# Performance work log

Hardware: AMD Instinct MI355X
Metric: run time of the kernel (lower is better)

Reference implementation:

```python
import jax, jax.numpy as jnp
import numpy as np


def setup_inputs() -> dict:
    key = jax.random.key(0)
    ks = jax.random.split(key, 6)
    Ci, Co, m1, m2 = 64, 64, 32, 32
    B, S = 16, 256
    inp = {
        "x": jax.random.normal(ks[0], (B, Ci, S, S), dtype=jnp.float32),
        "y0_r": jax.random.normal(ks[1], (Ci, Co, m1 - 1, 1), dtype=jnp.float32) * 0.02,
        "y0_i": jax.random.normal(ks[2], (Ci, Co, m1 - 1, 1), dtype=jnp.float32) * 0.02,
        "yposx_r": jax.random.normal(ks[3], (Ci, Co, 2 * m1 - 1, m2 - 1), dtype=jnp.float32) * 0.02,
        "yposx_i": jax.random.normal(ks[4], (Ci, Co, 2 * m1 - 1, m2 - 1), dtype=jnp.float32) * 0.02,
        "w00": jax.random.normal(ks[5], (Ci, Co, 1, 1), dtype=jnp.float32) * 0.02,
        "out_size": 256,
    }
    return inp


def _build_weights(y0_r, y0_i, yposx_r, yposx_i, w00):
    # torch: cat([y0, w00.cfloat(), y0.flip(-2).conj()], dim=-2) then cat with yposx on dim=-1
    y0 = y0_r + 1j * y0_i                      # [Ci,Co,m1-1,1]
    yposx = yposx_r + 1j * yposx_i             # [Ci,Co,2m1-1,m2-1]
    col0 = jnp.concatenate(
        [y0, w00.astype(jnp.complex64), jnp.conj(jnp.flip(y0, axis=-2))], axis=-2
    )                                           # [Ci,Co,2m1-1,1]
    return jnp.concatenate([col0, yposx], axis=-1)  # [Ci,Co,2m1-1,m2]


def reference(x, y0_r, y0_i, yposx_r, yposx_i, w00, out_size):
    m1 = y0_r.shape[-2] + 1
    m2 = yposx_r.shape[-1] + 1
    Co = y0_r.shape[1]
    B = x.shape[0]
    in_size = x.shape[-1]
    H = x.shape[-2]
    weights = _build_weights(y0_r, y0_i, yposx_r, yposx_i, w00)

    # index of zero frequency after fftshift (== N//2 for fftfreq of length N)
    f0_in = H // 2
    x_ft = jnp.fft.fftshift(jnp.fft.rfft2(x, norm="ortho"), axes=-2)
    x_ft = x_ft[..., f0_in - m1 + 1 : f0_in + m1, :m2]       # [B,Ci,2m1-1,m2]

    out_modes = jnp.einsum("bixy,ioxy->boxy", x_ft, weights)  # [B,Co,2m1-1,m2]

    f0_out = out_size // 2
    out_ft = jnp.zeros((B, Co, out_size, out_size // 2 + 1), dtype=jnp.complex64)
    out_ft = out_ft.at[..., f0_out - m1 + 1 : f0_out + m1, :m2].set(out_modes)

    y = jnp.fft.irfft2(
        jnp.fft.ifftshift(out_ft, axes=-2), s=(out_size, out_size), norm="ortho"
    ) * (out_size / in_size)
    return y.astype(jnp.float32)
```

## Files before the change

### kernel.cpp

```cpp
#include <hip/hip_runtime.h>


typedef __attribute__((ext_vector_type(8))) short bfrag8;
typedef __attribute__((ext_vector_type(4))) float facc4;

#define F1F_O 0u
#define T2F_O 16384u
#define T4F_O 81920u
#define F5F_O 147456u
#define WF_O  163840u
#define X1T_O 33193984u
#define C2_O  49971200u
#define X2M_O 54165504u
#define WTMP_O WF_O
#define C3_O  X1T_O
#define X3T_O (X1T_O + 4128768u)

#define TWO_PI_256 0.0245436926f

__device__ __forceinline__ unsigned short f2bf(float f) {
  unsigned u = __float_as_uint(f);
  u += 0x7fffu + ((u >> 16) & 1u);
  return (unsigned short)(u >> 16);
}
__device__ __forceinline__ bfrag8 ldf(const unsigned short* p) {
  return *(const bfrag8*)p;
}
__device__ __forceinline__ bfrag8 ld8u2(const unsigned short* p) {
  union { uint2 u2[2]; bfrag8 f; } v;
  v.u2[0] = *(const uint2*)(p);
  v.u2[1] = *(const uint2*)(p + 4);
  return v.f;
}

__global__ void k_tables(unsigned short* ws) {
  int t = threadIdx.x;
  for (int q = 0; q < 4; ++q) {
    int idx = blockIdx.x * 1024 + q * 256 + t;
    float val = 0.f; unsigned dst;
    if (idx < 16384) {
      int u = idx, j = u & 7, lane = (u >> 3) & 63, nt = (u >> 9) & 3, ks = u >> 11;
      int k = ks * 32 + (lane >> 4) * 8 + j, n = nt * 16 + (lane & 15);
      if (n < 32) val =  cosf((float)((k * n) & 255) * TWO_PI_256) * (1.f / 256.f);
      else        val = -sinf((float)((k * (n - 32)) & 255) * TWO_PI_256) * (1.f / 256.f);
      dst = F1F_O + (unsigned)idx;
    } else if (idx < 81920) {
      int u = idx - 16384, j = u & 7, lane = (u >> 3) & 63, ks = (u >> 9) & 15, mt = u >> 13;
      int m = mt * 16 + (lane & 15), k = ks * 32 + (lane >> 4) * 8 + j;
      if (m < 126) {
        int ky = m < 63 ? m : m - 63;
        int y = k & 255, f = (ky + 225) & 255;
        float ang = (float)((y * f) & 255) * TWO_PI_256;
        float c = cosf(ang), s = sinf(ang);
        val = (m < 63) ? ((k < 256) ? c : s) : ((k < 256) ? -s : c);
      }
      dst = T2F_O + (unsigned)u;
    } else if (idx < 147456) {
      int u = idx - 81920, j = u & 7, lane = (u >> 3) & 63, ks = (u >> 9) & 3, mt = u >> 11;
      int m = mt * 16 + (lane & 15), k = ks * 32 + (lane >> 4) * 8 + j;
      if (k < 126) {
        int ky = k < 63 ? k : k - 63;
        int y = m & 255, f = (ky + 225) & 255;
        float ang = (float)((y * f) & 255) * TWO_PI_256;
        float c = cosf(ang), s = sinf(ang);
        val = (m < 256) ? ((k < 63) ? c : -s) : ((k < 63) ? s : c);
      }
      dst = T4F_O + (unsigned)u;
    } else {
      int u = idx - 147456, j = u & 7, lane = (u >> 3) & 63, nt = (u >> 9) & 15, ks = u >> 13;
      int k = ks * 32 + (lane >> 4) * 8 + j, n = nt * 16 + (lane & 15);
      int kf = k & 31;
      float ang = (float)((kf * n) & 255) * TWO_PI_256;
      if (k < 32) val = ((kf == 0) ? 1.f : 2.f) * cosf(ang) * (1.f / 256.f);
      else        val = (kf == 0) ? 0.f : -2.f * sinf(ang) * (1.f / 256.f);
      dst = F5F_O + (unsigned)u;
    }
    ws[dst] = f2bf(val);
  }
}

__global__ void k_wpre(const float* __restrict__ y0r, const float* __restrict__ y0i,
                       const float* __restrict__ ypr, const float* __restrict__ ypi,
                       const float* __restrict__ w00, unsigned short* ws) {
  unsigned* Wtmp = (unsigned*)(ws + WTMP_O);
  int chunk = blockIdx.x >> 4, kq = blockIdx.x & 15;
  int io = chunk * 256 + threadIdx.x;
  int ky0 = kq * 4, nky = (kq == 15) ? 3 : 4;
  const float* pr = ypr + (size_t)io * 1953 + (size_t)ky0 * 31;
  const float* pi_ = ypi + (size_t)io * 1953 + (size_t)ky0 * 31;
  for (int q = 0; q < nky; ++q) {
    int ky = ky0 + q;
#pragma unroll
    for (int kxs = 0; kxs < 31; ++kxs) {
      float r = pr[q * 31 + kxs], im = pi_[q * 31 + kxs];
      Wtmp[(unsigned)(ky * 32 + kxs + 1) * 4096u + io] =
          (unsigned)f2bf(r) | ((unsigned)f2bf(im) << 16);
    }
  }
  if (kq == 0) {
    float rr[31], ii[31];
#pragma unroll
    for (int j = 0; j < 31; ++j) { rr[j] = y0r[io * 31 + j]; ii[j] = y0i[io * 31 + j]; }
    float w0 = w00[io];
    for (int ky = 0; ky < 63; ++ky) {
      float r, im;
      if (ky < 31)       { r = rr[ky];      im = ii[ky]; }
      else if (ky == 31) { r = w0;          im = 0.f; }
      else               { r = rr[62 - ky]; im = -ii[62 - ky]; }
      Wtmp[(unsigned)(ky * 32) * 4096u + io] =
          (unsigned)f2bf(r) | ((unsigned)f2bf(im) << 16);
    }
  }
}

__global__ void k_s1(const float* __restrict__ x, unsigned short* ws) {
  __shared__ unsigned short F1s[16384];
  __shared__ unsigned short As[128 * 40];
  const unsigned short* F1g = ws + F1F_O;
  unsigned short* X1t = ws + X1T_O;
  int t = threadIdx.x;
  int bi = blockIdx.x >> 1, y0 = (blockIdx.x & 1) * 128;
#pragma unroll
  for (int q = 0; q < 8; ++q)
    ((uint4*)F1s)[q * 256 + t] = ((const uint4*)F1g)[q * 256 + t];
  int lane = t & 63, w = t >> 6, quad = lane >> 4, nlo = lane & 15;
  int mt0 = w * 2;
  facc4 acc[2][4];
#pragma unroll
  for (int a = 0; a < 2; ++a)
#pragma unroll
    for (int b = 0; b < 4; ++b) acc[a][b] = (facc4){0.f, 0.f, 0.f, 0.f};
  const float* img = x + (size_t)bi * 65536 + (size_t)y0 * 256;
  for (int ks = 0; ks < 8; ++ks) {
    __syncthreads();
#pragma unroll
    for (int q = 0; q < 4; ++q) {
      int flat = q * 1024 + t * 4;
      int r = flat >> 5, cc = flat & 31;
      float4 v = *(const float4*)(img + r * 256 + ks * 32 + cc);
      unsigned short b4[4] = { f2bf(v.x), f2bf(v.y), f2bf(v.z), f2bf(v.w) };
      *(uint2*)(As + r * 40 + cc) = *(uint2*)b4;
    }
    __syncthreads();
    bfrag8 a0 = *(bfrag8*)(As + (mt0 * 16 + nlo) * 40 + quad * 8);
    bfrag8 a1 = *(bfrag8*)(As + ((mt0 + 1) * 16 + nlo) * 40 + quad * 8);
#pragma unroll
    for (int nt = 0; nt < 4; ++nt) {
      bfrag8 b = *(bfrag8*)(F1s + ((ks * 4 + nt) * 64 + lane) * 8);
      acc[0][nt] = __builtin_amdgcn_mfma_f32_16x16x32_bf16(a0, b, acc[0][nt], 0, 0, 0);
      acc[1][nt] = __builtin_amdgcn_mfma_f32_16x16x32_bf16(a1, b, acc[1][nt], 0, 0, 0);
    }
  }
#pragma unroll
  for (int ml = 0; ml < 2; ++ml)
#pragma unroll
    for (int nt = 0; nt < 4; ++nt) {
      facc4 v = acc[ml][nt];
      int ccol = nt * 16 + nlo, n = ccol & 31, half = ccol >> 5;
      int yrow = y0 + (mt0 + ml) * 16 + quad * 4;
      unsigned short pk[4] = { f2bf(v[0]), f2bf(v[1]), f2bf(v[2]), f2bf(v[3]) };
      *(uint2*)(X1t + (unsigned)bi * 16384u + n * 512 + half * 256 + yrow) = *(uint2*)pk;
    }
}

__global__ void k_s2(unsigned short* ws) {
  const unsigned short* T2f = ws + T2F_O;
  const unsigned short* X1t = ws + X1T_O;
  unsigned short* C2 = ws + C2_O;
  int t = threadIdx.x, lane = t & 63, w = t >> 6, quad = lane >> 4, nlo = lane & 15;
  int bi = blockIdx.x, mt0 = w * 2;
  facc4 acc[2][2];
#pragma unroll
  for (int a = 0; a < 2; ++a)
#pragma unroll
    for (int b = 0; b < 2; ++b) acc[a][b] = (facc4){0.f, 0.f, 0.f, 0.f};
  const unsigned short* Bb = X1t + (unsigned)bi * 16384u;
  for (int ks = 0; ks < 16; ++ks) {
    bfrag8 a0 = ldf(T2f + ((mt0 * 16 + ks) * 64 + lane) * 8);
    bfrag8 a1 = ldf(T2f + (((mt0 + 1) * 16 + ks) * 64 + lane) * 8);
    bfrag8 b0 = ldf(Bb + nlo * 512 + ks * 32 + quad * 8);
    bfrag8 b1 = ldf(Bb + (16 + nlo) * 512 + ks * 32 + quad * 8);
    acc[0][0] = __builtin_amdgcn_mfma_f32_16x16x32_bf16(a0, b0, acc[0][0], 0, 0, 0);
    acc[0][1] = __builtin_amdgcn_mfma_f32_16x16x32_bf16(a0, b1, acc[0][1], 0, 0, 0);
    acc[1][0] = __builtin_amdgcn_mfma_f32_16x16x32_bf16(a1, b0, acc[1][0], 0, 0, 0);
    acc[1][1] = __builtin_amdgcn_mfma_f32_16x16x32_bf16(a1, b1, acc[1][1], 0, 0, 0);
  }
#pragma unroll
  for (int ml = 0; ml < 2; ++ml)
#pragma unroll
    for (int nt = 0; nt < 2; ++nt) {
      facc4 v = acc[ml][nt];
      int n = nt * 16 + nlo, mb = (mt0 + ml) * 16 + quad * 4;
#pragma unroll
      for (int r = 0; r < 4; ++r)
        C2[(unsigned)bi * 4096u + (mb + r) * 32 + n] = f2bf(v[r]);
    }
}

__global__ void k_t1(unsigned short* ws) {
  __shared__ unsigned short lds[512 * 36];
  const unsigned short* C2 = ws + C2_O;
  unsigned short* X2m = ws + X2M_O;
  int ky = blockIdx.x >> 2, b0 = (blockIdx.x & 3) * 4;
  int t = threadIdx.x;
#pragma unroll
  for (int rr = 0; rr < 2; ++rr) {
    int R = rr * 256 + t;
    int half = R >> 8, bloc = (R >> 6) & 3, i = R & 63;
    const uint2* src2 = (const uint2*)(C2 + (unsigned)((b0 + bloc) * 64 + i) * 4096u
                                          + (half * 63 + ky) * 32);
    uint2* d2 = (uint2*)(lds + R * 36);
#pragma unroll
    for (int c = 0; c < 8; ++c) d2[c] = src2[c];
  }
  __syncthreads();
#pragma unroll
  for (int it = 0; it < 8; ++it) {
    int flat = (it * 256 + t) * 8;
    int kx = flat >> 9, bloc = (flat >> 7) & 3, ic0 = flat & 127;
    unsigned short outv[8];
#pragma unroll
    for (int j = 0; j < 8; ++j) {
      int ic = ic0 + j, i = ic & 63, half = ic >> 6;
      outv[j] = lds[(half * 256 + bloc * 64 + i) * 36 + kx];
    }
    *(uint4*)(X2m + (unsigned)(ky * 32 + kx) * 2048u + (b0 + bloc) * 128 + ic0) = *(uint4*)outv;
  }
}

__global__ void k_s3(unsigned short* ws) {
  __shared__ unsigned lds[64 * 65];
  const unsigned short* X2m = ws + X2M_O;
  const unsigned* Wtmp = (const unsigned*)(ws + WTMP_O);
  unsigned short* C3 = ws + C3_O;
  int t = threadIdx.x, lane = t & 63, w = t >> 6, quad = lane >> 4, nlo = lane & 15;
  int nt0 = w * 2;
  int mode = blockIdx.x;
#pragma unroll
  for (int q = 0; q < 4; ++q) {
    int io = q * 1024 + t * 4;
    uint4 vv = *(const uint4*)(Wtmp + (unsigned)mode * 4096u + io);
    unsigned base = (unsigned)(io >> 6) * 65u + (io & 63);
    lds[base] = vv.x; lds[base + 1] = vv.y; lds[base + 2] = vv.z; lds[base + 3] = vv.w;
  }
  __syncthreads();
  facc4 acc0 = (facc4){0.f, 0.f, 0.f, 0.f}, acc1 = acc0;
  const unsigned short* Am = X2m + (unsigned)mode * 2048u;
#pragma unroll
  for (int ks = 0; ks < 4; ++ks) {
    bfrag8 a = ldf(Am + nlo * 128 + ks * 32 + quad * 8);
    bfrag8 b0, b1;
#pragma unroll
    for (int f = 0; f < 2; ++f) {
      int n = (nt0 + f) * 16 + nlo, o = n & 63, oh = n >> 6;
#pragma unroll
      for (int j = 0; j < 8; ++j) {
        int i = (ks & 1) * 32 + quad * 8 + j;
        unsigned pk = lds[i * 65 + o];
        unsigned short re = (unsigned short)(pk & 0xffffu);
        unsigned short im = (unsigned short)(pk >> 16);
        unsigned short ev = (ks < 2) ? (oh == 0 ? re : im)
                                     : (oh == 0 ? (unsigned short)(im ^ 0x8000u) : re);
        if (f == 0) b0[j] = (short)ev; else b1[j] = (short)ev;
      }
    }
    acc0 = __builtin_amdgcn_mfma_f32_16x16x32_bf16(a, b0, acc0, 0, 0, 0);
    acc1 = __builtin_amdgcn_mfma_f32_16x16x32_bf16(a, b1, acc1, 0, 0, 0);
  }
  int bq = quad * 4;
#pragma unroll
  for (int r = 0; r < 4; ++r) {
    C3[(unsigned)mode * 2048u + (bq + r) * 128 + nt0 * 16 + nlo] = f2bf(acc0[r]);
    C3[(unsigned)mode * 2048u + (bq + r) * 128 + (nt0 + 1) * 16 + nlo] = f2bf(acc1[r]);
  }
}

__global__ void k_t2(unsigned short* ws) {
  __shared__ unsigned short lds[2 * 63 * 132];
  const unsigned short* C3 = ws + C3_O;
  unsigned short* X3t = ws + X3T_O;
  int kx = blockIdx.x >> 3, b0 = (blockIdx.x & 7) * 2;
  int t = threadIdx.x;
#pragma unroll
  for (int it = 0; it < 8; ++it) {
    int g = it * 256 + t;
    if (g < 2016) {
      int flat = g * 8;
      int ky = flat >> 8, bloc = (flat >> 7) & 1, nc0 = flat & 127;
      const uint2* src2 = (const uint2*)(C3 + (unsigned)(ky * 32 + kx) * 2048u
                                            + (b0 + bloc) * 128 + nc0);
      uint2* d2 = (uint2*)(lds + (bloc * 63 + ky) * 132 + nc0);
      d2[0] = src2[0]; d2[1] = src2[1];
    }
  }
  __syncthreads();
#pragma unroll
  for (int it = 0; it < 8; ++it) {
    int flat = (it * 256 + t) * 8;
    int bloc = flat >> 13, o = (flat >> 7) & 63, kk0 = flat & 127;
    unsigned short outv[8];
#pragma unroll
    for (int j = 0; j < 8; ++j) {
      int kk = kk0 + j;
      unsigned short v = 0;
      if (kk < 63)        v = lds[(bloc * 63 + kk) * 132 + o];
      else if (kk < 126)  v = lds[(bloc * 63 + (kk - 63)) * 132 + 64 + o];
      outv[j] = v;
    }
    int bo = (b0 + bloc) * 64 + o;
    *(uint4*)(X3t + (unsigned)bo * 4096u + kx * 128 + kk0) = *(uint4*)outv;
  }
}

__global__ void __launch_bounds__(256) k_s45(unsigned short* ws, float* __restrict__ out) {
  __shared__ unsigned short F5s[16384];
  __shared__ unsigned short Y1s[512 * 36];
  const unsigned short* T4f = ws + T4F_O;
  const unsigned short* X3t = ws + X3T_O;
  const unsigned short* F5g = ws + F5F_O;
  int t = threadIdx.x, lane = t & 63, w = t >> 6, quad = lane >> 4, nlo = lane & 15;
  int bo = blockIdx.x;
#pragma unroll
  for (int q = 0; q < 8; ++q)
    ((uint4*)F5s)[q * 256 + t] = ((const uint4*)F5g)[q * 256 + t];
  int mt0 = w * 8;
  facc4 acc[8][2];
#pragma unroll
  for (int ii = 0; ii < 8; ++ii)
#pragma unroll
    for (int bb = 0; bb < 2; ++bb) acc[ii][bb] = (facc4){0.f, 0.f, 0.f, 0.f};
  const unsigned short* Bb = X3t + (unsigned)bo * 4096u;
#pragma unroll
  for (int ks = 0; ks < 4; ++ks) {
    bfrag8 b0 = ldf(Bb + nlo * 128 + ks * 32 + quad * 8);
    bfrag8 b1 = ldf(Bb + (16 + nlo) * 128 + ks * 32 + quad * 8);
#pragma unroll
    for (int ml = 0; ml < 8; ++ml) {
      bfrag8 a = ldf(T4f + (((mt0 + ml) * 4 + ks) * 64 + lane) * 8);
      acc[ml][0] = __builtin_amdgcn_mfma_f32_16x16x32_bf16(a, b0, acc[ml][0], 0, 0, 0);
      acc[ml][1] = __builtin_amdgcn_mfma_f32_16x16x32_bf16(a, b1, acc[ml][1], 0, 0, 0);
    }
  }
#pragma unroll
  for (int ml = 0; ml < 8; ++ml)
#pragma unroll
    for (int nt = 0; nt < 2; ++nt) {
      facc4 v = acc[ml][nt];
      int m = (mt0 + ml) * 16 + quad * 4, n = nt * 16 + nlo;
#pragma unroll
      for (int r = 0; r < 4; ++r) Y1s[(m + r) * 36 + n] = f2bf(v[r]);
    }
  __syncthreads();
  int mt0b = w * 2;
  for (int sub = 0; sub < 4; ++sub) {
    int y0 = (sub >> 1) * 128, nh = sub & 1, x0 = nh * 128;
    facc4 acc5[2][8];
#pragma unroll
    for (int ii = 0; ii < 2; ++ii)
#pragma unroll
      for (int bb = 0; bb < 8; ++bb) acc5[ii][bb] = (facc4){0.f, 0.f, 0.f, 0.f};
#pragma unroll
    for (int ks = 0; ks < 2; ++ks) {
      bfrag8 a0 = ld8u2(Y1s + (ks * 256 + y0 + mt0b * 16 + nlo) * 36 + quad * 8);
      bfrag8 a1 = ld8u2(Y1s + (ks * 256 + y0 + (mt0b + 1) * 16 + nlo) * 36 + quad * 8);
#pragma unroll
      for (int nt = 0; nt < 8; ++nt) {
        bfrag8 b = *(bfrag8*)(F5s + ((ks * 16 + nh * 8 + nt) * 64 + lane) * 8);
        acc5[0][nt] = __builtin_amdgcn_mfma_f32_16x16x32_bf16(a0, b, acc5[0][nt], 0, 0, 0);
        acc5[1][nt] = __builtin_amdgcn_mfma_f32_16x16x32_bf16(a1, b, acc5[1][nt], 0, 0, 0);
      }
    }
    float* ob = out + (size_t)bo * 65536 + (size_t)y0 * 256 + x0;
#pragma unroll
    for (int ml = 0; ml < 2; ++ml)
#pragma unroll
      for (int nt = 0; nt < 8; ++nt) {
        int yr = (mt0b + ml) * 16 + quad * 4, xc = nt * 16 + nlo;
        facc4 v = acc5[ml][nt];
#pragma unroll
        for (int r = 0; r < 4; ++r) ob[(yr + r) * 256 + xc] = v[r];
      }
  }
}

extern "C" void kernel_launch(void* const* d_in, const int* in_sizes, int n_in,
                              void* d_out, int out_size, void* d_ws, size_t ws_size,
                              hipStream_t stream) {
  (void)in_sizes; (void)n_in; (void)out_size; (void)ws_size;
  const float* x   = (const float*)d_in[0];
  const float* y0r = (const float*)d_in[1];
  const float* y0i = (const float*)d_in[2];
  const float* ypr = (const float*)d_in[3];
  const float* ypi = (const float*)d_in[4];
  const float* w00 = (const float*)d_in[5];
  unsigned short* ws = (unsigned short*)d_ws;
  float* out = (float*)d_out;

  k_tables<<<dim3(160),  dim3(256), 0, stream>>>(ws);
  k_wpre  <<<dim3(256),  dim3(256), 0, stream>>>(y0r, y0i, ypr, ypi, w00, ws);
  k_s1    <<<dim3(2048), dim3(256), 0, stream>>>(x, ws);
  k_s2    <<<dim3(1024), dim3(256), 0, stream>>>(ws);
  k_t1    <<<dim3(252),  dim3(256), 0, stream>>>(ws);
  k_s3    <<<dim3(2016), dim3(256), 0, stream>>>(ws);
  k_t2    <<<dim3(256),  dim3(256), 0, stream>>>(ws);
  k_s45   <<<dim3(1024), dim3(256), 0, stream>>>(ws, out);
}
```

Measured before the change: 610.8 us.

## Fuse forward DFT stages and fold transposes into scattered stores

Merges the row-DFT and column-DFT stages into one kernel that keeps the intermediate image spectrum in shared memory instead of a global round trip. The two transpose kernels are removed: the fused kernel and the mode-mixing kernel write their outputs straight into the layouts the next stage expects. This uses scalar scattered stores. The zero padding of the inverse input is moved into the weight-prep kernel. The aim is to cut launches and global intermediate traffic, at the cost of uncoalesced 2-byte stores and more shared memory per block.

New measurement: 609.0 us. No clear change (-0.3%).

```diff
diff --git a/kernel.cpp b/kernel.cpp
--- a/kernel.cpp
+++ b/kernel.cpp
@@ -8,13 +8,9 @@
 #define T2F_O 16384u
 #define T4F_O 81920u
 #define F5F_O 147456u
-#define WF_O  163840u
-#define X1T_O 33193984u
-#define C2_O  49971200u
+#define WTMP_O 163840u
+#define X3T_O 37322752u
 #define X2M_O 54165504u
-#define WTMP_O WF_O
-#define C3_O  X1T_O
-#define X3T_O (X1T_O + 4128768u)
 
 #define TWO_PI_256 0.0245436926f
 
@@ -83,6 +79,12 @@
                        const float* __restrict__ ypr, const float* __restrict__ ypi,
                        const float* __restrict__ w00, unsigned short* ws) {
   unsigned* Wtmp = (unsigned*)(ws + WTMP_O);
+  {
+    unsigned short* X3t = ws + X3T_O;
+    int g = blockIdx.x * 256 + threadIdx.x;
+    int bo = g >> 6, kx = (g >> 1) & 31, kk = 126 + (g & 1);
+    X3t[(unsigned)bo * 4096u + kx * 128 + kk] = 0;
+  }
   int chunk = blockIdx.x >> 4, kq = blockIdx.x & 15;
   int io = chunk * 256 + threadIdx.x;
   int ky0 = kq * 4, nky = (kq == 15) ? 3 : 4;
@@ -113,129 +115,101 @@
   }
 }
 
-__global__ void k_s1(const float* __restrict__ x, unsigned short* ws) {
+__global__ void __launch_bounds__(256) k_s12(const float* __restrict__ x, unsigned short* ws) {
   __shared__ unsigned short F1s[16384];
   __shared__ unsigned short As[128 * 40];
+  __shared__ unsigned short X1ls[32 * 528];
   const unsigned short* F1g = ws + F1F_O;
-  unsigned short* X1t = ws + X1T_O;
+  const unsigned short* T2f = ws + T2F_O;
+  unsigned short* X2m = ws + X2M_O;
   int t = threadIdx.x;
-  int bi = blockIdx.x >> 1, y0 = (blockIdx.x & 1) * 128;
+  int bi = blockIdx.x;
+  int b = bi >> 6, ii = bi & 63;
 #pragma unroll
   for (int q = 0; q < 8; ++q)
     ((uint4*)F1s)[q * 256 + t] = ((const uint4*)F1g)[q * 256 + t];
   int lane = t & 63, w = t >> 6, quad = lane >> 4, nlo = lane & 15;
   int mt0 = w * 2;
-  facc4 acc[2][4];
+  for (int y0 = 0; y0 < 256; y0 += 128) {
+    facc4 acc[2][4];
+#pragma unroll
+    for (int a = 0; a < 2; ++a)
+#pragma unroll
+      for (int bb = 0; bb < 4; ++bb) acc[a][bb] = (facc4){0.f, 0.f, 0.f, 0.f};
+    const float* img = x + (size_t)bi * 65536 + (size_t)y0 * 256;
+    for (int ks = 0; ks < 8; ++ks) {
+      __syncthreads();
+#pragma unroll
+      for (int q = 0; q < 4; ++q) {
+        int flat = q * 1024 + t * 4;
+        int r = flat >> 5, cc = flat & 31;
+        float4 v = *(const float4*)(img + r * 256 + ks * 32 + cc);
+        unsigned short b4[4] = { f2bf(v.x), f2bf(v.y), f2bf(v.z), f2bf(v.w) };
+        *(uint2*)(As + r * 40 + cc) = *(uint2*)b4;
+      }
+      __syncthreads();
+      bfrag8 a0 = *(bfrag8*)(As + (mt0 * 16 + nlo) * 40 + quad * 8);
+      bfrag8 a1 = *(bfrag8*)(As + ((mt0 + 1) * 16 + nlo) * 40 + quad * 8);
+#pragma unroll
+      for (int nt = 0; nt < 4; ++nt) {
+        bfrag8 bfr = *(bfrag8*)(F1s + ((ks * 4 + nt) * 64 + lane) * 8);
+        acc[0][nt] = __builtin_amdgcn_mfma_f32_16x16x32_bf16(a0, bfr, acc[0][nt], 0, 0, 0);
+        acc[1][nt] = __builtin_amdgcn_mfma_f32_16x16x32_bf16(a1, bfr, acc[1][nt], 0, 0, 0);
+      }
+    }
+#pragma unroll
+    for (int ml = 0; ml < 2; ++ml)
+#pragma unroll
+      for (int nt = 0; nt < 4; ++nt) {
+        facc4 v = acc[ml][nt];
+        int ccol = nt * 16 + nlo, n = ccol & 31, half = ccol >> 5;
+        int yrow = y0 + (mt0 + ml) * 16 + quad * 4;
+        unsigned short pk[4] = { f2bf(v[0]), f2bf(v[1]), f2bf(v[2]), f2bf(v[3]) };
+        *(uint2*)(X1ls + n * 528 + half * 256 + yrow) = *(uint2*)pk;
+      }
+  }
+  __syncthreads();
+  facc4 c2[2][2];
 #pragma unroll
   for (int a = 0; a < 2; ++a)
 #pragma unroll
-    for (int b = 0; b < 4; ++b) acc[a][b] = (facc4){0.f, 0.f, 0.f, 0.f};
-  const float* img = x + (size_t)bi * 65536 + (size_t)y0 * 256;
-  for (int ks = 0; ks < 8; ++ks) {
-    __syncthreads();
-#pragma unroll
-    for (int q = 0; q < 4; ++q) {
-      int flat = q * 1024 + t * 4;
-      int r = flat >> 5, cc = flat & 31;
-      float4 v = *(const float4*)(img + r * 256 + ks * 32 + cc);
-      unsigned short b4[4] = { f2bf(v.x), f2bf(v.y), f2bf(v.z), f2bf(v.w) };
-      *(uint2*)(As + r * 40 + cc) = *(uint2*)b4;
-    }
-    __syncthreads();
-    bfrag8 a0 = *(bfrag8*)(As + (mt0 * 16 + nlo) * 40 + quad * 8);
-    bfrag8 a1 = *(bfrag8*)(As + ((mt0 + 1) * 16 + nlo) * 40 + quad * 8);
-#pragma unroll
-    for (int nt = 0; nt < 4; ++nt) {
-      bfrag8 b = *(bfrag8*)(F1s + ((ks * 4 + nt) * 64 + lane) * 8);
-      acc[0][nt] = __builtin_amdgcn_mfma_f32_16x16x32_bf16(a0, b, acc[0][nt], 0, 0, 0);
-      acc[1][nt] = __builtin_amdgcn_mfma_f32_16x16x32_bf16(a1, b, acc[1][nt], 0, 0, 0);
-    }
-  }
-#pragma unroll
-  for (int ml = 0; ml < 2; ++ml)
-#pragma unroll
-    for (int nt = 0; nt < 4; ++nt) {
-      facc4 v = acc[ml][nt];
-      int ccol = nt * 16 + nlo, n = ccol & 31, half = ccol >> 5;
-      int yrow = y0 + (mt0 + ml) * 16 + quad * 4;
-      unsigned short pk[4] = { f2bf(v[0]), f2bf(v[1]), f2bf(v[2]), f2bf(v[3]) };
-      *(uint2*)(X1t + (unsigned)bi * 16384u + n * 512 + half * 256 + yrow) = *(uint2*)pk;
-    }
-}
-
-__global__ void k_s2(unsigned short* ws) {
-  const unsigned short* T2f = ws + T2F_O;
-  const unsigned short* X1t = ws + X1T_O;
-  unsigned short* C2 = ws + C2_O;
-  int t = threadIdx.x, lane = t & 63, w = t >> 6, quad = lane >> 4, nlo = lane & 15;
-  int bi = blockIdx.x, mt0 = w * 2;
-  facc4 acc[2][2];
-#pragma unroll
-  for (int a = 0; a < 2; ++a)
-#pragma unroll
-    for (int b = 0; b < 2; ++b) acc[a][b] = (facc4){0.f, 0.f, 0.f, 0.f};
-  const unsigned short* Bb = X1t + (unsigned)bi * 16384u;
+    for (int bb = 0; bb < 2; ++bb) c2[a][bb] = (facc4){0.f, 0.f, 0.f, 0.f};
   for (int ks = 0; ks < 16; ++ks) {
     bfrag8 a0 = ldf(T2f + ((mt0 * 16 + ks) * 64 + lane) * 8);
     bfrag8 a1 = ldf(T2f + (((mt0 + 1) * 16 + ks) * 64 + lane) * 8);
-    bfrag8 b0 = ldf(Bb + nlo * 512 + ks * 32 + quad * 8);
-    bfrag8 b1 = ldf(Bb + (16 + nlo) * 512 + ks * 32 + quad * 8);
-    acc[0][0] = __builtin_amdgcn_mfma_f32_16x16x32_bf16(a0, b0, acc[0][0], 0, 0, 0);
-    acc[0][1] = __builtin_amdgcn_mfma_f32_16x16x32_bf16(a0, b1, acc[0][1], 0, 0, 0);
-    acc[1][0] = __builtin_amdgcn_mfma_f32_16x16x32_bf16(a1, b0, acc[1][0], 0, 0, 0);
-    acc[1][1] = __builtin_amdgcn_mfma_f32_16x16x32_bf16(a1, b1, acc[1][1], 0, 0, 0);
+    bfrag8 b0 = *(bfrag8*)(X1ls + nlo * 528 + ks * 32 + quad * 8);
+    bfrag8 b1 = *(bfrag8*)(X1ls + (16 + nlo) * 528 + ks * 32 + quad * 8);
+    c2[0][0] = __builtin_amdgcn_mfma_f32_16x16x32_bf16(a0, b0, c2[0][0], 0, 0, 0);
+    c2[0][1] = __builtin_amdgcn_mfma_f32_16x16x32_bf16(a0, b1, c2[0][1], 0, 0, 0);
+    c2[1][0] = __builtin_amdgcn_mfma_f32_16x16x32_bf16(a1, b0, c2[1][0], 0, 0, 0);
+    c2[1][1] = __builtin_amdgcn_mfma_f32_16x16x32_bf16(a1, b1, c2[1][1], 0, 0, 0);
   }
 #pragma unroll
   for (int ml = 0; ml < 2; ++ml)
 #pragma unroll
     for (int nt = 0; nt < 2; ++nt) {
-      facc4 v = acc[ml][nt];
+      facc4 v = c2[ml][nt];
       int n = nt * 16 + nlo, mb = (mt0 + ml) * 16 + quad * 4;
 #pragma unroll
-      for (int r = 0; r < 4; ++r)
-        C2[(unsigned)bi * 4096u + (mb + r) * 32 + n] = f2bf(v[r]);
-    }
-}
-
-__global__ void k_t1(unsigned short* ws) {
-  __shared__ unsigned short lds[512 * 36];
-  const unsigned short* C2 = ws + C2_O;
-  unsigned short* X2m = ws + X2M_O;
-  int ky = blockIdx.x >> 2, b0 = (blockIdx.x & 3) * 4;
-  int t = threadIdx.x;
-#pragma unroll
-  for (int rr = 0; rr < 2; ++rr) {
-    int R = rr * 256 + t;
-    int half = R >> 8, bloc = (R >> 6) & 3, i = R & 63;
-    const uint2* src2 = (const uint2*)(C2 + (unsigned)((b0 + bloc) * 64 + i) * 4096u
-                                          + (half * 63 + ky) * 32);
-    uint2* d2 = (uint2*)(lds + R * 36);
-#pragma unroll
-    for (int c = 0; c < 8; ++c) d2[c] = src2[c];
-  }
-  __syncthreads();
-#pragma unroll
-  for (int it = 0; it < 8; ++it) {
-    int flat = (it * 256 + t) * 8;
-    int kx = flat >> 9, bloc = (flat >> 7) & 3, ic0 = flat & 127;
-    unsigned short outv[8];
-#pragma unroll
-    for (int j = 0; j < 8; ++j) {
-      int ic = ic0 + j, i = ic & 63, half = ic >> 6;
-      outv[j] = lds[(half * 256 + bloc * 64 + i) * 36 + kx];
-    }
-    *(uint4*)(X2m + (unsigned)(ky * 32 + kx) * 2048u + (b0 + bloc) * 128 + ic0) = *(uint4*)outv;
-  }
+      for (int r = 0; r < 4; ++r) {
+        int m = mb + r;
+        if (m < 126) {
+          int hf = (m >= 63) ? 1 : 0, ky = m - hf * 63;
+          X2m[(unsigned)(ky * 32 + n) * 2048u + b * 128 + hf * 64 + ii] = f2bf(v[r]);
+        }
+      }
+    }
 }
 
 __global__ void k_s3(unsigned short* ws) {
   __shared__ unsigned lds[64 * 65];
   const unsigned short* X2m = ws + X2M_O;
   const unsigned* Wtmp = (const unsigned*)(ws + WTMP_O);
-  unsigned short* C3 = ws + C3_O;
+  unsigned short* X3t = ws + X3T_O;
   int t = threadIdx.x, lane = t & 63, w = t >> 6, quad = lane >> 4, nlo = lane & 15;
   int nt0 = w * 2;
   int mode = blockIdx.x;
+  int kyM = mode >> 5, kxM = mode & 31;
 #pragma unroll
   for (int q = 0; q < 4; ++q) {
     int io = q * 1024 + t * 4;
@@ -270,45 +244,15 @@
   int bq = quad * 4;
 #pragma unroll
   for (int r = 0; r < 4; ++r) {
-    C3[(unsigned)mode * 2048u + (bq + r) * 128 + nt0 * 16 + nlo] = f2bf(acc0[r]);
-    C3[(unsigned)mode * 2048u + (bq + r) * 128 + (nt0 + 1) * 16 + nlo] = f2bf(acc1[r]);
-  }
-}
-
-__global__ void k_t2(unsigned short* ws) {
-  __shared__ unsigned short lds[2 * 63 * 132];
-  const unsigned short* C3 = ws + C3_O;
-  unsigned short* X3t = ws + X3T_O;
-  int kx = blockIdx.x >> 3, b0 = (blockIdx.x & 7) * 2;
-  int t = threadIdx.x;
-#pragma unroll
-  for (int it = 0; it < 8; ++it) {
-    int g = it * 256 + t;
-    if (g < 2016) {
-      int flat = g * 8;
-      int ky = flat >> 8, bloc = (flat >> 7) & 1, nc0 = flat & 127;
-      const uint2* src2 = (const uint2*)(C3 + (unsigned)(ky * 32 + kx) * 2048u
-                                            + (b0 + bloc) * 128 + nc0);
-      uint2* d2 = (uint2*)(lds + (bloc * 63 + ky) * 132 + nc0);
-      d2[0] = src2[0]; d2[1] = src2[1];
-    }
-  }
-  __syncthreads();
-#pragma unroll
-  for (int it = 0; it < 8; ++it) {
-    int flat = (it * 256 + t) * 8;
-    int bloc = flat >> 13, o = (flat >> 7) & 63, kk0 = flat & 127;
-    unsigned short outv[8];
-#pragma unroll
-    for (int j = 0; j < 8; ++j) {
-      int kk = kk0 + j;
-      unsigned short v = 0;
-      if (kk < 63)        v = lds[(bloc * 63 + kk) * 132 + o];
-      else if (kk < 126)  v = lds[(bloc * 63 + (kk - 63)) * 132 + 64 + o];
-      outv[j] = v;
-    }
-    int bo = (b0 + bloc) * 64 + o;
-    *(uint4*)(X3t + (unsigned)bo * 4096u + kx * 128 + kk0) = *(uint4*)outv;
+    int bb = bq + r;
+    {
+      int nc = nt0 * 16 + nlo, o = nc & 63, hf = nc >> 6;
+      X3t[(unsigned)(bb * 64 + o) * 4096u + kxM * 128 + hf * 63 + kyM] = f2bf(acc0[r]);
+    }
+    {
+      int nc = (nt0 + 1) * 16 + nlo, o = nc & 63, hf = nc >> 6;
+      X3t[(unsigned)(bb * 64 + o) * 4096u + kxM * 128 + hf * 63 + kyM] = f2bf(acc1[r]);
+    }
   }
 }
 
@@ -326,9 +270,9 @@
   int mt0 = w * 8;
   facc4 acc[8][2];
 #pragma unroll
-  for (int ii = 0; ii < 8; ++ii)
-#pragma unroll
-    for (int bb = 0; bb < 2; ++bb) acc[ii][bb] = (facc4){0.f, 0.f, 0.f, 0.f};
+  for (int a = 0; a < 8; ++a)
+#pragma unroll
+    for (int bb = 0; bb < 2; ++bb) acc[a][bb] = (facc4){0.f, 0.f, 0.f, 0.f};
   const unsigned short* Bb = X3t + (unsigned)bo * 4096u;
 #pragma unroll
   for (int ks = 0; ks < 4; ++ks) {
@@ -352,34 +296,41 @@
     }
   __syncthreads();
   int mt0b = w * 2;
-  for (int sub = 0; sub < 4; ++sub) {
-    int y0 = (sub >> 1) * 128, nh = sub & 1, x0 = nh * 128;
-    facc4 acc5[2][8];
-#pragma unroll
-    for (int ii = 0; ii < 2; ++ii)
-#pragma unroll
-      for (int bb = 0; bb < 8; ++bb) acc5[ii][bb] = (facc4){0.f, 0.f, 0.f, 0.f};
+  for (int yh = 0; yh < 2; ++yh) {
+    int y0 = yh * 128;
+    bfrag8 a0[2], a1[2];
 #pragma unroll
     for (int ks = 0; ks < 2; ++ks) {
-      bfrag8 a0 = ld8u2(Y1s + (ks * 256 + y0 + mt0b * 16 + nlo) * 36 + quad * 8);
-      bfrag8 a1 = ld8u2(Y1s + (ks * 256 + y0 + (mt0b + 1) * 16 + nlo) * 36 + quad * 8);
-#pragma unroll
-      for (int nt = 0; nt < 8; ++nt) {
-        bfrag8 b = *(bfrag8*)(F5s + ((ks * 16 + nh * 8 + nt) * 64 + lane) * 8);
-        acc5[0][nt] = __builtin_amdgcn_mfma_f32_16x16x32_bf16(a0, b, acc5[0][nt], 0, 0, 0);
-        acc5[1][nt] = __builtin_amdgcn_mfma_f32_16x16x32_bf16(a1, b, acc5[1][nt], 0, 0, 0);
-      }
-    }
-    float* ob = out + (size_t)bo * 65536 + (size_t)y0 * 256 + x0;
-#pragma unroll
-    for (int ml = 0; ml < 2; ++ml)
-#pragma unroll
-      for (int nt = 0; nt < 8; ++nt) {
-        int yr = (mt0b + ml) * 16 + quad * 4, xc = nt * 16 + nlo;
-        facc4 v = acc5[ml][nt];
-#pragma unroll
-        for (int r = 0; r < 4; ++r) ob[(yr + r) * 256 + xc] = v[r];
-      }
+      a0[ks] = ld8u2(Y1s + (ks * 256 + y0 + mt0b * 16 + nlo) * 36 + quad * 8);
+      a1[ks] = ld8u2(Y1s + (ks * 256 + y0 + (mt0b + 1) * 16 + nlo) * 36 + quad * 8);
+    }
+    for (int nh = 0; nh < 2; ++nh) {
+      int x0 = nh * 128;
+      facc4 acc5[2][8];
+#pragma unroll
+      for (int a = 0; a < 2; ++a)
+#pragma unroll
+        for (int bb = 0; bb < 8; ++bb) acc5[a][bb] = (facc4){0.f, 0.f, 0.f, 0.f};
+#pragma unroll
+      for (int ks = 0; ks < 2; ++ks) {
+#pragma unroll
+        for (int nt = 0; nt < 8; ++nt) {
+          bfrag8 bfr = *(bfrag8*)(F5s + ((ks * 16 + nh * 8 + nt) * 64 + lane) * 8);
+          acc5[0][nt] = __builtin_amdgcn_mfma_f32_16x16x32_bf16(a0[ks], bfr, acc5[0][nt], 0, 0, 0);
+          acc5[1][nt] = __builtin_amdgcn_mfma_f32_16x16x32_bf16(a1[ks], bfr, acc5[1][nt], 0, 0, 0);
+        }
+      }
+      float* ob = out + (size_t)bo * 65536 + (size_t)y0 * 256 + x0;
+#pragma unroll
+      for (int ml = 0; ml < 2; ++ml)
+#pragma unroll
+        for (int nt = 0; nt < 8; ++nt) {
+          int yr = (mt0b + ml) * 16 + quad * 4, xc = nt * 16 + nlo;
+          facc4 v = acc5[ml][nt];
+#pragma unroll
+          for (int r = 0; r < 4; ++r) ob[(yr + r) * 256 + xc] = v[r];
+        }
+    }
   }
 }
 
@@ -398,10 +349,7 @@
 
   k_tables<<<dim3(160),  dim3(256), 0, stream>>>(ws);
   k_wpre  <<<dim3(256),  dim3(256), 0, stream>>>(y0r, y0i, ypr, ypi, w00, ws);
-  k_s1    <<<dim3(2048), dim3(256), 0, stream>>>(x, ws);
-  k_s2    <<<dim3(1024), dim3(256), 0, stream>>>(ws);
-  k_t1    <<<dim3(252),  dim3(256), 0, stream>>>(ws);
+  k_s12   <<<dim3(1024), dim3(256), 0, stream>>>(x, ws);
   k_s3    <<<dim3(2016), dim3(256), 0, stream>>>(ws);
-  k_t2    <<<dim3(256),  dim3(256), 0, stream>>>(ws);
   k_s45   <<<dim3(1024), dim3(256), 0, stream>>>(ws, out);
 }
```
